# Kernel optimization log

Hardware: AMD Instinct MI355X
Metric: run time of the kernel (lower is better)

## Reference

```python
import jax, jax.numpy as jnp
import numpy as np

# ---- quantization constants (8-bit, per-tensor affine; representative values) ----
Q_MAX = 255.0
S_IN, Z_IN = 0.05, 128.0      # block input
S1, Z1 = 0.04, 128.0          # after expand 1x1 + hardswish
S2, Z2 = 0.04, 128.0          # after depthwise 5x5 + hardswish
S_SE1, Z_SE1 = 0.03, 128.0    # SE fc1 output
S_SE2, Z_SE2 = 1.0 / 255.0, 0.0  # SE fc2 hardsigmoid output in [0,1]
S_MUL, Z_MUL = 0.04, 128.0    # SE gated activation
S3, Z3 = 0.05, 128.0          # after project 1x1
S_OUT, Z_OUT = 0.06, 128.0    # after residual add
W_SCALE = 0.01                # symmetric per-tensor weight scale (zero_point = 0)
EXP_C = 576                   # expanded channels (depthwise groups)


def conv(x, w, stride=1, padding=0, groups=1):
    return jax.lax.conv_general_dilated(
        x, w, (stride, stride), [(padding, padding), (padding, padding)],
        feature_group_count=groups, dimension_numbers=('NCHW', 'OIHW', 'NCHW'))


def hardswish(x):
    return x * jnp.clip(x + 3.0, 0.0, 6.0) * (1.0 / 6.0)


def hardsigmoid(x):
    return jnp.clip(x + 3.0, 0.0, 6.0) * (1.0 / 6.0)


def qconv(x_q, w_q, b_q, s_in, z_in, s_out, z_out, stride=1, padding=0, groups=1, act=None):
    """Quantized conv: int-domain accumulation (simulated in fp32), fused activation
    on the dequantized accumulator, then requantize to [0, Q_MAX]."""
    acc = conv(x_q - z_in, w_q, stride, padding, groups) + b_q[None, :, None, None]
    deq = acc * (s_in * W_SCALE)  # dequantize accumulator
    if act == 'hardswish':
        deq = hardswish(deq)
    elif act == 'hardsigmoid':
        deq = hardsigmoid(deq)
    return jnp.clip(deq * (1.0 / s_out) + z_out, 0.0, Q_MAX)


def setup_inputs() -> dict:
    key = jax.random.key(0)
    ks = jax.random.split(key, 11)
    def qw(k, shape):  # int8-style symmetric weights stored as fp32 integers
        return jnp.round(jnp.clip(jax.random.normal(k, shape) * 40.0, -127.0, 127.0))
    def qb(k, n):      # int32-style bias in accumulator domain
        return jnp.round(jax.random.normal(k, (n,)) * 500.0)
    return {
        'x':      jnp.round(jax.random.uniform(ks[0], (64, 96, 28, 28)) * Q_MAX),
        'w_exp':  qw(ks[1], (576, 96, 1, 1)),  'b_exp':  qb(ks[2], 576),
        'w_dw':   qw(ks[3], (576, 1, 5, 5)),   'b_dw':   qb(ks[4], 576),
        'w_se1':  qw(ks[5], (144, 576, 1, 1)), 'b_se1':  qb(ks[6], 144),
        'w_se2':  qw(ks[7], (576, 144, 1, 1)), 'b_se2':  qb(ks[8], 576),
        'w_proj': qw(ks[9], (96, 576, 1, 1)),  'b_proj': qb(ks[10], 96),
    }


def reference(x, w_exp, b_exp, w_dw, b_dw, w_se1, b_se1, w_se2, b_se2, w_proj, b_proj):
    # expand 1x1 (+ hardswish)
    e = qconv(x, w_exp, b_exp, S_IN, Z_IN, S1, Z1, act='hardswish')
    # depthwise 5x5, padding=(5-1)//2=2, groups=expanded (+ hardswish)
    d = qconv(e, w_dw, b_dw, S1, Z1, S2, Z2, padding=2, groups=EXP_C, act='hardswish')
    # squeeze-excitation: global avg pool -> fc1 -> fc2(hardsigmoid) -> quantized mul
    pooled = jnp.mean(d, axis=(2, 3), keepdims=True)  # [N, 576, 1, 1]
    g1 = qconv(pooled, w_se1, b_se1, S2, Z2, S_SE1, Z_SE1)
    g2 = qconv(g1, w_se2, b_se2, S_SE1, Z_SE1, S_SE2, Z_SE2, act='hardsigmoid')
    gated = jnp.clip((g2 - Z_SE2) * (d - Z2) * (S_SE2 * S2 / S_MUL) + Z_MUL, 0.0, Q_MAX)
    # project 1x1 (linear)
    p = qconv(gated, w_proj, b_proj, S_MUL, Z_MUL, S3, Z3)
    # quantized residual add (stride=1, in==out channels -> use_res_connect)
    out = jnp.clip((x - Z_IN) * (S_IN / S_OUT) + (p - Z3) * (S3 / S_OUT) + Z_OUT, 0.0, Q_MAX)
    return out
```

## Files before the change

### kernel.cpp

```cpp
#include <hip/hip_runtime.h>

typedef _Float16 v8h __attribute__((ext_vector_type(8)));
typedef _Float16 v4h __attribute__((ext_vector_type(4)));
typedef _Float16 v2h __attribute__((ext_vector_type(2)));
typedef float v4f __attribute__((ext_vector_type(4)));

#define NB 64
#define CI 96
#define CE 576
#define CO 96
#define HW 784
#define SEC 144

#if defined(__has_builtin)
#if __has_builtin(__builtin_amdgcn_fdot2)
#define HAVE_FDOT2 1
#endif
#endif

__device__ __forceinline__ float fdot2(v2h a, v2h b, float c) {
#ifdef HAVE_FDOT2
  return __builtin_amdgcn_fdot2(a, b, c, false);
#else
  return (float)a[0] * (float)b[0] + ((float)a[1] * (float)b[1] + c);
#endif
}

__device__ __forceinline__ float clampf(float x, float lo, float hi) {
#if defined(__has_builtin)
#if __has_builtin(__builtin_amdgcn_fmed3f)
  return __builtin_amdgcn_fmed3f(x, lo, hi);
#else
  return fminf(fmaxf(x, lo), hi);
#endif
#else
  return fminf(fmaxf(x, lo), hi);
#endif
}

__global__ __launch_bounds__(256) void k0_pack_cvt(const float* __restrict__ x,
                                                   _Float16* __restrict__ x_f,
                                                   const float* __restrict__ w_exp,
                                                   const float* __restrict__ w_proj,
                                                   _Float16* __restrict__ w_exp_h,
                                                   _Float16* __restrict__ w_proj_h) {
  __shared__ _Float16 xl[112][104];
  const int tid = threadIdx.x;

  if (blockIdx.y == NB) {
    for (int i = blockIdx.x * 256 + tid; i < CE * CI; i += 7 * 256) {
      w_exp_h[i]  = (_Float16)w_exp[i];
      w_proj_h[i] = (_Float16)w_proj[i];
    }
    return;
  }

  const int n = blockIdx.y;
  const int hw0 = blockIdx.x * 112;

  for (int idx = tid; idx < CI * 28; idx += 256) {
    int c = idx / 28, seg = idx % 28;
    const float4 v = *(const float4*)&x[(n * CI + c) * HW + hw0 + seg * 4];
    int row = seg * 4;
    xl[row + 0][c] = (_Float16)(v.x - 128.0f);
    xl[row + 1][c] = (_Float16)(v.y - 128.0f);
    xl[row + 2][c] = (_Float16)(v.z - 128.0f);
    xl[row + 3][c] = (_Float16)(v.w - 128.0f);
  }
  __syncthreads();

  for (int idx = tid; idx < 1344; idx += 256) {
    int t_l = idx / 192, rem = idx % 192, s = rem / 64, ln = rem % 64;
    int hw_l = t_l * 16 + (ln & 15), ci = s * 32 + (ln >> 4) * 8;
    v8h o;
#pragma unroll
    for (int j = 0; j < 8; ++j) o[j] = xl[hw_l][ci + j];
    size_t t = (size_t)(blockIdx.x * 7 + t_l);
    *(v8h*)&x_f[(((size_t)n * 49 + t) * 3 + s) * 512 + ln * 8] = o;
  }
}

__global__ __launch_bounds__(512, 8) void k12_fused(const _Float16* __restrict__ x_f,
                                                    const _Float16* __restrict__ w_exp_h,
                                                    const float* __restrict__ b_exp,
                                                    const float* __restrict__ w_dw,
                                                    const float* __restrict__ b_dw,
                                                    _Float16* __restrict__ d_t,
                                                    float* __restrict__ d_sums2) {
  __shared__ _Float16 e_lds[16][18][38];
  __shared__ _Float16 d_tile[16][392];
  __shared__ _Float16 w_pairs[16][5][8];
  const int tid = threadIdx.x;
  const int n = blockIdx.z;
  const int h = blockIdx.y;
  const int c0 = blockIdx.x * 16;

  {
    unsigned long long* z = (unsigned long long*)&e_lds[0][0][0];
    for (int idx = tid; idx < 16 * 18 * 38 * 2 / 8; idx += 512) z[idx] = 0ull;
  }
  for (int idx = tid; idx < 640; idx += 512) {
    int c = idx / 40, r = idx % 40, dy = r / 8, k = r % 8;
    int tap = (k < 4) ? k : (k - 3);
    w_pairs[c][dy][k] = (_Float16)w_dw[(c0 + c) * 25 + dy * 5 + tap];
  }
  __syncthreads();

  const int wv = tid >> 6, lane = tid & 63;
  const int l15 = lane & 15, q = lane >> 4;

  {
    const _Float16* wrow = &w_exp_h[(c0 + l15) * CI + q * 8];
    v8h a0 = *(const v8h*)(wrow);
    v8h a1 = *(const v8h*)(wrow + 32);
    v8h a2 = *(const v8h*)(wrow + 64);
    float bia3[4], bia2[4];
#pragma unroll
    for (int r = 0; r < 4; ++r) {
      float b = b_exp[c0 + q * 4 + r];
      bia3[r] = fmaf(b, 5.0e-4f, 3.0f);
      bia2[r] = b * (5.0e-4f * 25.0f / 6.0f);
    }

    const int ir0 = 14 * h - 2;
    const _Float16* xb = x_f + (size_t)n * (49 * 3 * 512) + lane * 8;
    int hw0 = (21 * h + wv) * 16 + l15;
    int y = hw0 / 28;
    int xx = hw0 - y * 28;
#pragma unroll
    for (int it = 0; it < 4; ++it) {
      int t_l = wv + it * 8;
      if (t_l < 28) {
        int t = 21 * h + t_l;
        const _Float16* xt = xb + (size_t)t * (3 * 512);
        v8h b0 = *(const v8h*)(xt);
        v8h b1 = *(const v8h*)(xt + 512);
        v8h b2 = *(const v8h*)(xt + 1024);
        v4f acc = (v4f){0.f, 0.f, 0.f, 0.f};
        acc = __builtin_amdgcn_mfma_f32_16x16x32_f16(a0, b0, acc, 0, 0, 0);
        acc = __builtin_amdgcn_mfma_f32_16x16x32_f16(a1, b1, acc, 0, 0, 0);
        acc = __builtin_amdgcn_mfma_f32_16x16x32_f16(a2, b2, acc, 0, 0, 0);
        _Float16* dst = &e_lds[q * 4][y - ir0][6 + xx];
#pragma unroll
        for (int r = 0; r < 4; ++r) {
          float t1  = fmaf(acc[r], 5.0e-4f, bia3[r]);
          float cl  = clampf(t1, 0.0f, 6.0f);
          float a2v = fmaf(acc[r], 5.0e-4f * 25.0f / 6.0f, bia2[r]);
          float ev  = clampf(a2v * cl, -128.0f, 127.0f);
          dst[r * (18 * 38)] = (_Float16)ev;
        }
      }
      xx += 16; y += 4;
      if (xx >= 28) { xx -= 28; ++y; }
    }
  }
  __syncthreads();

  const int c = tid >> 5, l = tid & 31;
  v2h W01[5], W23[5], W12[5], W34[5];
  float W0s[5], W4s[5];
#pragma unroll
  for (int dy = 0; dy < 5; ++dy) {
    W01[dy] = *(const v2h*)&w_pairs[c][dy][0];
    W23[dy] = *(const v2h*)&w_pairs[c][dy][2];
    W12[dy] = *(const v2h*)&w_pairs[c][dy][4];
    W34[dy] = *(const v2h*)&w_pairs[c][dy][6];
    W0s[dy] = (float)W01[dy][0];
    W4s[dy] = (float)W34[dy][1];
  }
  const float bc = b_dw[c0 + c];

#define DW_REQUANT(oo, dvv)                                                   \
  {                                                                           \
    float t1_ = fmaf((oo), 4.0e-4f, 3.0f);                                    \
    float cl_ = clampf(t1_, 0.0f, 6.0f);                                      \
    dvv = clampf((oo) * (4.0e-4f * 25.0f / 6.0f) * cl_, -128.0f, 127.0f);     \
  }

  float csum = 0.0f;
  if (l < 28) {
    const int ry = l >> 1;
    const int bx = (l & 1) * 14;
    v2h P0[5], P1[5], P2[5], P3[5];
#pragma unroll
    for (int dy = 0; dy < 5; ++dy) {
      const _Float16* row = &e_lds[c][ry + dy][bx];
      P0[dy] = *(const v2h*)(row + 4);
      P1[dy] = *(const v2h*)(row + 6);
      P2[dy] = *(const v2h*)(row + 8);
      P3[dy] = *(const v2h*)(row + 10);
    }
#pragma unroll
    for (int xi = 0; xi < 3; ++xi) {
      const int x0 = bx + xi * 4;
      float o0 = bc, o1 = bc, o2 = bc, o3 = bc;
#pragma unroll
      for (int dy = 0; dy < 5; ++dy) {
        o0 = fdot2(P0[dy], W01[dy], o0);
        o0 = fdot2(P1[dy], W23[dy], o0);
        o0 += (float)P2[dy][0] * W4s[dy];
        o1 += (float)P0[dy][1] * W0s[dy];
        o1 = fdot2(P1[dy], W12[dy], o1);
        o1 = fdot2(P2[dy], W34[dy], o1);
        o2 = fdot2(P1[dy], W01[dy], o2);
        o2 = fdot2(P2[dy], W23[dy], o2);
        o2 += (float)P3[dy][0] * W4s[dy];
        o3 += (float)P1[dy][1] * W0s[dy];
        o3 = fdot2(P2[dy], W12[dy], o3);
        o3 = fdot2(P3[dy], W34[dy], o3);
      }
      float d0, d1, d2, d3;
      DW_REQUANT(o0, d0); DW_REQUANT(o1, d1);
      DW_REQUANT(o2, d2); DW_REQUANT(o3, d3);
      csum += (d0 + d1) + (d2 + d3);
      v2h dva, dvb;
      dva[0] = (_Float16)d0; dva[1] = (_Float16)d1;
      dvb[0] = (_Float16)d2; dvb[1] = (_Float16)d3;
      *(v2h*)&d_tile[c][ry * 28 + x0]     = dva;
      *(v2h*)&d_tile[c][ry * 28 + x0 + 2] = dvb;
#pragma unroll
      for (int dy = 0; dy < 5; ++dy) {
        const _Float16* row = &e_lds[c][ry + dy][bx];
        P0[dy] = P2[dy];
        P1[dy] = P3[dy];
        P2[dy] = *(const v2h*)(row + x0 - bx + 12);
        P3[dy] = *(const v2h*)(row + x0 - bx + 14);
      }
    }
    {
      float o0 = bc, o1 = bc;
#pragma unroll
      for (int dy = 0; dy < 5; ++dy) {
        o0 = fdot2(P0[dy], W01[dy], o0);
        o0 = fdot2(P1[dy], W23[dy], o0);
        o0 += (float)P2[dy][0] * W4s[dy];
        o1 += (float)P0[dy][1] * W0s[dy];
        o1 = fdot2(P1[dy], W12[dy], o1);
        o1 = fdot2(P2[dy], W34[dy], o1);
      }
      float d0, d1;
      DW_REQUANT(o0, d0); DW_REQUANT(o1, d1);
      csum += d0 + d1;
      v2h dv; dv[0] = (_Float16)d0; dv[1] = (_Float16)d1;
      *(v2h*)&d_tile[c][ry * 28 + bx + 12] = dv;
    }
  }
#pragma unroll
  for (int m = 16; m >= 1; m >>= 1) csum += __shfl_xor(csum, m);
  if (l == 0) d_sums2[((size_t)h * NB + n) * CE + c0 + c] = csum;

  __syncthreads();
  const size_t obase = ((size_t)n * 72 + (c0 >> 3)) * 784 + 392 * h;
  if (tid < 392) {
    int hw_l = tid;
    v8h o0, o1;
#pragma unroll
    for (int j = 0; j < 8; ++j) { o0[j] = d_tile[j][hw_l]; o1[j] = d_tile[8 + j][hw_l]; }
    *(v8h*)&d_t[(obase + hw_l) * 8] = o0;
    *(v8h*)&d_t[(obase + 784 + hw_l) * 8] = o1;
  }
}

__global__ __launch_bounds__(256) void k3a_fc1(const float* __restrict__ d_sums2,
                                               const float* __restrict__ w_se1,
                                               const float* __restrict__ b_se1,
                                               float* __restrict__ g1) {
  const int tid = threadIdx.x;
  const int wv = tid >> 6, lane = tid & 63;
  const int n = blockIdx.y;
  const int o = blockIdx.x * 4 + wv;
  const float* wrow = &w_se1[o * CE];
  const float* s0 = &d_sums2[(size_t)n * CE];
  const float* s1 = &d_sums2[((size_t)NB + n) * CE];
  float p = 0.f;
#pragma unroll
  for (int s = 0; s < 9; ++s) {
    int cc = lane + s * 64;
    p = fmaf(wrow[cc], s0[cc] + s1[cc], p);
  }
#pragma unroll
  for (int m = 32; m >= 1; m >>= 1) p += __shfl_xor(p, m);
  if (lane == 0) {
    g1[n * SEC + o] = clampf(fmaf(p, 1.0f / 58800.0f,
                                  fmaf(b_se1[o], 1.0f / 75.0f, 128.0f)),
                             0.0f, 255.0f) - 128.0f;
  }
}

__global__ __launch_bounds__(256) void k3b_fc2(const float* __restrict__ g1,
                                               const float* __restrict__ w_se2,
                                               const float* __restrict__ b_se2,
                                               _Float16* __restrict__ g2h) {
  const int tid = threadIdx.x;
  const int wv = tid >> 6, lane = tid & 63;
  const int n = blockIdx.y;
  const int o = blockIdx.x * 4 + wv;
  const float* wrow = &w_se2[o * SEC];
  const float* grow = &g1[n * SEC];
  float p = fmaf(wrow[lane], grow[lane], wrow[lane + 64] * grow[lane + 64]);
  if (lane < 16) p = fmaf(wrow[lane + 128], grow[lane + 128], p);
#pragma unroll
  for (int m = 32; m >= 1; m >>= 1) p += __shfl_xor(p, m);
  if (lane == 0) {
    float t = fmaf(p, 3.0e-4f, fmaf(b_se2[o], 3.0e-4f, 3.0f));
    g2h[n * CE + o] = (_Float16)(clampf(t, 0.0f, 6.0f) * (1.0f / 6.0f));
  }
}

__global__ __launch_bounds__(192) void k4_proj(const _Float16* __restrict__ d_t,
                                               const _Float16* __restrict__ g2h,
                                               const _Float16* __restrict__ w_proj_h,
                                               const float* __restrict__ b_proj,
                                               const float* __restrict__ x,
                                               float* __restrict__ out) {
  const int tid = threadIdx.x;
  const int n = blockIdx.z;
  const int co0 = blockIdx.y * 48;
  const int hw0 = blockIdx.x * 112;
  const int wv = tid >> 6, lane = tid & 63;
  const int l15 = lane & 15, q = lane >> 4;

  v4f acc[7];
#pragma unroll
  for (int t = 0; t < 7; ++t) acc[t] = (v4f){0.f, 0.f, 0.f, 0.f};

  const _Float16* dbase = d_t + (((size_t)n * 72 + q) * 784 + hw0 + l15) * 8;
  const _Float16* abase = &w_proj_h[(co0 + wv * 16 + l15) * CE + q * 8];
  const _Float16* gbase = &g2h[(size_t)n * CE + q * 8];

  for (int ks = 0; ks < 18; ++ks) {
    v8h a = *(const v8h*)(abase + ks * 32);
    v8h g = *(const v8h*)(gbase + ks * 32);
    v8h ag = a * g;
    const _Float16* dk = dbase + (size_t)ks * (4 * 784 * 8);
#pragma unroll
    for (int t = 0; t < 7; ++t) {
      v8h b = *(const v8h*)(dk + t * (16 * 8));
      acc[t] = __builtin_amdgcn_mfma_f32_16x16x32_f16(ag, b, acc[t], 0, 0, 0);
    }
  }

  float biaf[4];
#pragma unroll
  for (int r = 0; r < 4; ++r)
    biaf[r] = fmaf(b_proj[co0 + wv * 16 + q * 4 + r], 8.0e-3f, 128.0f);

#pragma unroll
  for (int t = 0; t < 7; ++t) {
#pragma unroll
    for (int r = 0; r < 4; ++r) {
      int co = co0 + wv * 16 + q * 4 + r;
      int hw = hw0 + t * 16 + l15;
      float p  = clampf(fmaf(acc[t][r], 8.0e-3f, biaf[r]), 0.0f, 255.0f);
      float xv = x[(n * CO + co) * HW + hw];
      float o = fmaf(xv + p, 0.8333333333f, -85.33333333f);
      out[(n * CO + co) * HW + hw] = clampf(o, 0.0f, 255.0f);
    }
  }
}

extern "C" void kernel_launch(void* const* d_in, const int* in_sizes, int n_in,
                              void* d_out, int out_size, void* d_ws, size_t ws_size,
                              hipStream_t stream) {
  const float* x      = (const float*)d_in[0];
  const float* w_exp  = (const float*)d_in[1];
  const float* b_exp  = (const float*)d_in[2];
  const float* w_dw   = (const float*)d_in[3];
  const float* b_dw   = (const float*)d_in[4];
  const float* w_se1  = (const float*)d_in[5];
  const float* b_se1  = (const float*)d_in[6];
  const float* w_se2  = (const float*)d_in[7];
  const float* b_se2  = (const float*)d_in[8];
  const float* w_proj = (const float*)d_in[9];
  const float* b_proj = (const float*)d_in[10];
  float* out = (float*)d_out;

  char* ws = (char*)d_ws;
  const size_t SZ_W  = (size_t)CE * CI * 2;
  const size_t SZ_XF = (size_t)NB * 49 * 3 * 512 * 2;
  const size_t SZ_D  = (size_t)NB * CE * HW * 2;
  const size_t SZ_S2 = (size_t)2 * NB * CE * 4;
  const size_t SZ_S  = (size_t)NB * CE * 4;
  _Float16* w_exp_h  = (_Float16*)(ws);
  _Float16* w_proj_h = (_Float16*)(ws + SZ_W);
  _Float16* x_f      = (_Float16*)(ws + 2 * SZ_W);
  _Float16* d_t      = (_Float16*)(ws + 2 * SZ_W + SZ_XF);
  float*    d_sums2  = (float*)   (ws + 2 * SZ_W + SZ_XF + SZ_D);
  float*    g1       = (float*)   (ws + 2 * SZ_W + SZ_XF + SZ_D + SZ_S2);
  _Float16* g2h      = (_Float16*)(ws + 2 * SZ_W + SZ_XF + SZ_D + SZ_S2 + SZ_S);

  k0_pack_cvt<<<dim3(7, NB + 1), 256, 0, stream>>>(x, x_f, w_exp, w_proj, w_exp_h, w_proj_h);
  k12_fused<<<dim3(36, 2, NB), 512, 0, stream>>>(x_f, w_exp_h, b_exp, w_dw, b_dw, d_t, d_sums2);
  k3a_fc1<<<dim3(36, NB), 256, 0, stream>>>(d_sums2, w_se1, b_se1, g1);
  k3b_fc2<<<dim3(144, NB), 256, 0, stream>>>(g1, w_se2, b_se2, g2h);
  k4_proj<<<dim3(7, 2, NB), 192, 0, stream>>>(d_t, g2h, w_proj_h, b_proj, x, out);
}
```

Before: 175.3 us.

## Remap blocks per XCD, pad LDS tile, double-buffer proj loads

Both fused kernels now remap the flat block index so that each XCD handles a contiguous group of batch images, which keeps each image's data in one XCD's L2. The d_tile LDS row is padded from 392 to 394 to reduce bank conflicts. The projection kernel's K loop is software-pipelined with two register buffers, loading the next slice while MFMAs run on the current one. This raises register use and could lower occupancy.

```diff
diff --git a/kernel.cpp b/kernel.cpp
--- a/kernel.cpp
+++ b/kernel.cpp
@@ -88,12 +88,16 @@
                                                     _Float16* __restrict__ d_t,
                                                     float* __restrict__ d_sums2) {
   __shared__ _Float16 e_lds[16][18][38];
-  __shared__ _Float16 d_tile[16][392];
+  __shared__ _Float16 d_tile[16][394];
   __shared__ _Float16 w_pairs[16][5][8];
   const int tid = threadIdx.x;
-  const int n = blockIdx.z;
-  const int h = blockIdx.y;
-  const int c0 = blockIdx.x * 16;
+
+  const int flat = blockIdx.x + 36 * blockIdx.y + 72 * blockIdx.z;
+  const int xcd = flat & 7, slot = flat >> 3;
+  const int nl = slot / 72, w72 = slot - nl * 72;
+  const int n = xcd * 8 + nl;
+  const int h = w72 / 36;
+  const int c0 = (w72 - h * 36) * 16;
 
   {
     unsigned long long* z = (unsigned long long*)&e_lds[0][0][0];
@@ -314,9 +318,15 @@
                                                const float* __restrict__ x,
                                                float* __restrict__ out) {
   const int tid = threadIdx.x;
-  const int n = blockIdx.z;
-  const int co0 = blockIdx.y * 48;
-  const int hw0 = blockIdx.x * 112;
+
+  const int flat = blockIdx.x + 7 * blockIdx.y + 14 * blockIdx.z;
+  const int xcd = flat & 7, slot = flat >> 3;
+  const int nl = slot / 14, w14 = slot - nl * 14;
+  const int n = xcd * 8 + nl;
+  const int byy = w14 / 7;
+  const int co0 = byy * 48;
+  const int hw0 = (w14 - byy * 7) * 112;
+
   const int wv = tid >> 6, lane = tid & 63;
   const int l15 = lane & 15, q = lane >> 4;
 
@@ -328,16 +338,32 @@
   const _Float16* abase = &w_proj_h[(co0 + wv * 16 + l15) * CE + q * 8];
   const _Float16* gbase = &g2h[(size_t)n * CE + q * 8];
 
-  for (int ks = 0; ks < 18; ++ks) {
-    v8h a = *(const v8h*)(abase + ks * 32);
-    v8h g = *(const v8h*)(gbase + ks * 32);
-    v8h ag = a * g;
-    const _Float16* dk = dbase + (size_t)ks * (4 * 784 * 8);
-#pragma unroll
-    for (int t = 0; t < 7; ++t) {
-      v8h b = *(const v8h*)(dk + t * (16 * 8));
-      acc[t] = __builtin_amdgcn_mfma_f32_16x16x32_f16(ag, b, acc[t], 0, 0, 0);
-    }
+#define K4_LOAD(SUF, KS)                                                      \
+  {                                                                           \
+    const int ks_ = (KS);                                                     \
+    a##SUF = *(const v8h*)(abase + ks_ * 32);                                 \
+    g##SUF = *(const v8h*)(gbase + ks_ * 32);                                 \
+    const _Float16* dk_ = dbase + (size_t)ks_ * (4 * 784 * 8);                \
+    _Pragma("unroll")                                                         \
+    for (int t = 0; t < 7; ++t) b##SUF[t] = *(const v8h*)(dk_ + t * (16 * 8));\
+  }
+#define K4_COMPUTE(SUF)                                                       \
+  {                                                                           \
+    v8h ag_ = a##SUF * g##SUF;                                                \
+    _Pragma("unroll")                                                         \
+    for (int t = 0; t < 7; ++t)                                               \
+      acc[t] = __builtin_amdgcn_mfma_f32_16x16x32_f16(ag_, b##SUF[t],         \
+                                                      acc[t], 0, 0, 0);       \
+  }
+
+  v8h aA, gA, bA[7], aB, gB, bB[7];
+  K4_LOAD(A, 0);
+#pragma unroll
+  for (int ks = 0; ks < 18; ks += 2) {
+    K4_LOAD(B, ks + 1);
+    K4_COMPUTE(A);
+    if (ks + 2 < 18) K4_LOAD(A, ks + 2);
+    K4_COMPUTE(B);
   }
 
   float biaf[4];
```

Result: faster. 171.2 us (-2.3%).
